# Kernel optimization log

Hardware: AMD Instinct MI355X
Metric: run time of the kernel (lower is better)

Reference implementation:

```python
import jax, jax.numpy as jnp
import numpy as np

B, K, U = 4096, 512, 3
P, LIFT, HID, NSUB = 5, 32, 128, 10
RATE_LO, RATE_HI = 0.01, 3.0
BASAL_LO, BASAL_HI = 0.0, 0.3


def _xavier(key, shape):
    fan_in, fan_out = shape[1], shape[0]
    lim = np.sqrt(6.0 / (fan_in + fan_out))
    return jax.random.uniform(key, shape, jnp.float32, -lim, lim)


def setup_inputs() -> dict:
    key = jax.random.key(0)
    ks = jax.random.split(key, 10)
    return {
        "y0": jax.random.uniform(ks[0], (B, P), jnp.float32),
        "u_seq": jax.random.uniform(ks[1], (B, K, U), jnp.float32),
        "dt_seq": jax.random.uniform(ks[2], (B, K), jnp.float32),
        # lift: Linear(in_u+P -> LIFT)
        "Wl": _xavier(ks[3], (LIFT, U + P)),
        "bl": jnp.zeros((LIFT,), jnp.float32),
        # GRU (single layer): weight_ih (3H, LIFT), weight_hh (3H, H)
        "W_ih": _xavier(ks[4], (3 * HID, LIFT)),
        "b_ih": jnp.zeros((3 * HID,), jnp.float32),
        "W_hh": _xavier(ks[5], (3 * HID, HID)),
        "b_hh": jnp.zeros((3 * HID,), jnp.float32),
        # head: Linear(H -> 13)
        "Wh": _xavier(ks[6], (13, HID)),
        "bh": jnp.zeros((13,), jnp.float32),
        # bolus-to-state jump matrix (in_u, P)
        "u_to_y_jump": 0.1 * jax.random.uniform(ks[7], (U, P), jnp.float32),
    }


def _rhs(y, theta):
    # y: (B,5) [A,D,G,J,M]; theta: (B,13) [kf1..4, kr1..4, kj1..5]
    A, D, G, J, M = (y[:, i] for i in range(5))
    kf1, kf2, kf3, kf4, kr1, kr2, kr3, kr4, kj1, kj2, kj3, kj4, kj5 = (
        theta[:, i] for i in range(13))
    dA = -kf1 * A + kr1 * D + kj1
    dD = kf1 * A - kr1 * D - kf2 * D + kr2 * G + kj2
    dG = kf2 * D - kr2 * G - kf3 * G + kr3 * J + kj3
    dJ = kf3 * G - kr3 * J - kf4 * J + kr4 * M + kj4
    dM = kf4 * J - kr4 * M + kj5
    return jnp.stack([dA, dD, dG, dJ, dM], axis=-1)


def _rk4(y, h, theta):
    # h: (B,1) substep size
    k1 = _rhs(y, theta)
    k2 = _rhs(y + 0.5 * h * k1, theta)
    k3 = _rhs(y + 0.5 * h * k2, theta)
    k4 = _rhs(y + h * k3, theta)
    return jnp.maximum(y + h / 6.0 * (k1 + 2.0 * k2 + 2.0 * k3 + k4), 0.0)


def reference(y0, u_seq, dt_seq, Wl, bl, W_ih, b_ih, W_hh, b_hh, Wh, bh, u_to_y_jump):
    Bb = y0.shape[0]
    hid = W_hh.shape[1]

    def step(carry, inp):
        y_prev, hst = carry
        u_k, dt_k = inp  # (B,U), (B,)
        feat = jnp.concatenate([u_k, jax.lax.stop_gradient(y_prev)], axis=-1)
        x = jax.nn.silu(feat @ Wl.T + bl)
        # PyTorch GRUCell math
        gx = x @ W_ih.T + b_ih
        gh = hst @ W_hh.T + b_hh
        gxr, gxz, gxn = jnp.split(gx, 3, axis=-1)
        ghr, ghz, ghn = jnp.split(gh, 3, axis=-1)
        r = jax.nn.sigmoid(gxr + ghr)
        zg = jax.nn.sigmoid(gxz + ghz)
        n = jnp.tanh(gxn + r * ghn)
        h_new = (1.0 - zg) * n + zg * hst
        raw = h_new @ Wh.T + bh
        rates = RATE_LO + (RATE_HI - RATE_LO) * jax.nn.sigmoid(raw[:, 0:8])
        basal = BASAL_LO + (BASAL_HI - BASAL_LO) * jax.nn.sigmoid(raw[:, 8:13])
        theta = jnp.concatenate([rates, basal], axis=-1)
        y = y_prev + u_k @ u_to_y_jump
        hsub = (dt_k / float(NSUB))[:, None]
        for _ in range(NSUB):
            y = _rk4(y, hsub, theta)
        return (y, h_new), (y, theta)

    y_init = y0 + 0.01
    h0 = jnp.zeros((Bb, hid), dtype=y0.dtype)
    # scan over time: (K,B,...)
    _, (ys, thetas) = jax.lax.scan(
        step, (y_init, h0), (u_seq.transpose(1, 0, 2), dt_seq.T))
    y_out = ys.transpose(1, 0, 2)        # (B,K,P)
    theta_out = thetas.transpose(1, 0, 2)  # (B,K,13)
    return y_out, theta_out
```

## Files before the change

### kernel.cpp

```cpp
#include <hip/hip_runtime.h>
#include <cstdint>
#include <cstddef>


#define KTOT 512
#define BB   16

typedef _Float16 half8 __attribute__((ext_vector_type(8)));
typedef float    f32x4 __attribute__((ext_vector_type(4)));

struct __align__(16) Smem {
  _Float16 hf16[BB][136];
  _Float16 xls[BB][32];
  float brz[256];
  float bnx[128];
  float bnh[128];
  float bhv[16];
  float theta[BB][14];
  float yst[BB][8];
  float ust[2][BB][4];
  float dtst[2][BB];
};

__device__ __forceinline__ float sigm(float x)     { return 1.f / (1.f + __expf(-x)); }
__device__ __forceinline__ float tanhfast(float x) { return 1.f - 2.f / (1.f + __expf(2.f * x)); }

template<int CTRL>
__device__ __forceinline__ float dppf(float x) {
  return __int_as_float(__builtin_amdgcn_mov_dpp(__float_as_int(x), CTRL, 0xf, 0xf, true));
}
#define QP_PLUS  0x39
#define QP_MINUS 0x93
#define QB0 0x00
#define QB1 0x55
#define QB2 0xAA
#define QB3 0xFF

#define MATMUL(Yr, Y4r, Xr, X4r, ALPHA) do {                                  \
  float xm_[5], xp_[5];                                                       \
  _Pragma("unroll")                                                           \
  for (int j_ = 0; j_ < 5; j_++) {                                            \
    xm_[j_] = dppf<QP_MINUS>(Xr[j_]);                                         \
    xp_[j_] = dppf<QP_PLUS >(Xr[j_]);                                         \
  }                                                                           \
  _Pragma("unroll")                                                           \
  for (int j_ = 0; j_ < 5; j_++) {                                            \
    const float ac_ = Zl*xm_[j_] + Zd*Xr[j_] + Zu*xp_[j_] + Zu4*X4r[j_];      \
    const float a4_ = Z43*Xr[j_] + Z44*X4r[j_];                               \
    Yr[j_]  = ((j_ == s_) ? 1.f : 0.f) + (ALPHA)*ac_;                         \
    Y4r[j_] = ((j_ == 4 ) ? 1.f : 0.f) + (ALPHA)*a4_;                         \
  } } while (0)

__global__ __launch_bounds__(512, 2) void rnn_scan_kernel(
    const float* __restrict__ y0,    const float* __restrict__ u_seq,
    const float* __restrict__ dt_sq, const float* __restrict__ Wl,
    const float* __restrict__ bl,    const float* __restrict__ W_ih,
    const float* __restrict__ b_ih,  const float* __restrict__ W_hh,
    const float* __restrict__ b_hh,  const float* __restrict__ Wh,
    const float* __restrict__ bh,    const float* __restrict__ jmp,
    float* __restrict__ y_out, float* __restrict__ th_out)
{
  __shared__ Smem sm;
  const int t   = threadIdx.x;
  const int w   = t >> 6;
  const int l   = t & 63;
  const int n16 = l & 15;
  const int q   = l >> 4;
  const int B0  = blockIdx.x * BB;

  if (t < 256) sm.brz[t] = b_ih[t] + b_hh[t];
  if (t < 128) { sm.bnx[t] = b_ih[256+t]; sm.bnh[t] = b_hh[256+t]; }
  if (t < 16)  sm.bhv[t] = (t < 13) ? bh[t] : 0.f;
  if (t >= 256 && t < 384) { const int b = (t-256) >> 3, i = (t-256) & 7;
    sm.yst[b][i] = (i < 5) ? (y0[(size_t)(B0+b)*5 + i] + 0.01f) : 0.f; }
  if (t >= 384 && t < 432) { const int b = (t-384)/3, c = (t-384) - ((t-384)/3)*3;
    sm.ust[0][b][c] = u_seq[((size_t)(B0+b)*KTOT + 0)*3 + c]; }
  if (t >= 432 && t < 448) sm.dtst[0][t-432] = dt_sq[(size_t)(B0+(t-432))*KTOT + 0];

  const int lb = t >> 5;
  const int lo = t & 31;
  float wlc[8];
  #pragma unroll
  for (int c = 0; c < 8; c++) wlc[c] = Wl[lo*8 + c];
  const float blv = bl[lo];

  half8 whf[4];
  #pragma unroll
  for (int ks = 0; ks < 4; ks++)
    #pragma unroll
    for (int i = 0; i < 8; i++) {
      const int kk = ks*32 + q*8 + i;
      whf[ks][i] = (n16 < 13) ? (_Float16)Wh[n16*128 + kk] : (_Float16)0.f;
    }

  const int jR = w*16 + n16;
  const int jZ = jR + 128, jN = jR + 256;
  half8 wihR, wihZ, wihN, whhR[4], whhZ[4], whhN[4];
  #pragma unroll
  for (int i = 0; i < 8; i++) {
    const int kk = q*8 + i;
    wihR[i] = (_Float16)W_ih[jR*32 + kk];
    wihZ[i] = (_Float16)W_ih[jZ*32 + kk];
    wihN[i] = (_Float16)W_ih[jN*32 + kk];
  }
  #pragma unroll
  for (int ks = 0; ks < 4; ks++)
    #pragma unroll
    for (int i = 0; i < 8; i++) {
      const int kk = ks*32 + q*8 + i;
      whhR[ks][i] = (_Float16)W_hh[jR*128 + kk];
      whhZ[ks][i] = (_Float16)W_hh[jZ*128 + kk];
      whhN[ks][i] = (_Float16)W_hh[jN*128 + kk];
    }

  float hreg[4] = {0.f, 0.f, 0.f, 0.f};
  const f32x4 zero4 = {0.f, 0.f, 0.f, 0.f};
  f32x4 accPreR = zero4, accPreZ = zero4, accPreN = zero4;

  const int s_ = l & 3, b4 = l >> 2;
  const float jr0 = jmp[0*5 + s_], jr1 = jmp[1*5 + s_], jr2 = jmp[2*5 + s_];
  const float j40 = (s_==3) ? jmp[4]  : 0.f;
  const float j41 = (s_==3) ? jmp[9]  : 0.f;
  const float j42 = (s_==3) ? jmp[14] : 0.f;

  const int yb = t/5, yi = t - (t/5)*5;
  float* yo_base = y_out + ((size_t)(B0 + (yb & 15))*KTOT)*5 + yi;
  const int ts = (t >= 80) ? (t - 80) : 0;
  const int tb = ts/13, tn = ts - (ts/13)*13;
  float* th_base = th_out + ((size_t)(B0 + (tb & 15))*KTOT)*13 + tn;
  const int upb = l/3, upc = l - (l/3)*3;

  __syncthreads();

  const float br  = sm.brz[jR];
  const float bz  = sm.brz[128 + jR];
  const float bx  = sm.bnx[jR];
  const float bn  = sm.bnh[jR];
  const float bb_ = sm.bhv[n16];

  #pragma unroll 1
  for (int k = 0; k < KTOT; k++) {
    const int buf  = k & 1;
    const int nbuf = (k + 1) & 1;
    const int kp   = (k + 1 < KTOT) ? (k + 1) : (KTOT - 1);

    {
      const f32x4 uu = *(const f32x4*)&sm.ust[buf][lb][0];
      const f32x4 ya = *(const f32x4*)&sm.yst[lb][0];
      const f32x4 yc = *(const f32x4*)&sm.yst[lb][4];
      const float a = blv
        + uu[0]*wlc[0] + uu[1]*wlc[1] + uu[2]*wlc[2]
        + ya[0]*wlc[3] + ya[1]*wlc[4] + ya[2]*wlc[5] + ya[3]*wlc[6]
        + yc[0]*wlc[7];
      sm.xls[lb][lo] = (_Float16)(a * sigm(a));
    }
    __syncthreads();

    if (k > 0) {
      if (t < 80)        yo_base[(size_t)(k-1)*5]  = sm.yst[yb][yi];
      else if (t < 288)  th_base[(size_t)(k-1)*13] = sm.theta[tb][tn];
    }
    {
      const half8 xf = *(const half8*)&sm.xls[n16][q*8];
      const f32x4 accR  = __builtin_amdgcn_mfma_f32_16x16x32_f16(xf, wihR, accPreR, 0,0,0);
      const f32x4 accZ  = __builtin_amdgcn_mfma_f32_16x16x32_f16(xf, wihZ, accPreZ, 0,0,0);
      const f32x4 accXN = __builtin_amdgcn_mfma_f32_16x16x32_f16(xf, wihN, zero4,   0,0,0);
      #pragma unroll
      for (int rg = 0; rg < 4; rg++) {
        const float r  = sigm(accR[rg] + br);
        const float z  = sigm(accZ[rg] + bz);
        const float nn = tanhfast(accXN[rg] + bx + r*(accPreN[rg] + bn));
        const float ho = hreg[rg];
        const float hn = nn + z*(ho - nn);
        hreg[rg] = hn;
        sm.hf16[q*4 + rg][jR] = (_Float16)hn;
      }
    }
    __syncthreads();

    float pref_u = 0.f, pref_dt = 0.f;
    if (w == 1 && l < 48)
      pref_u = u_seq[((size_t)(B0 + upb)*KTOT + kp)*3 + upc];
    if (w == 2 && l < 16)
      pref_dt = dt_sq[(size_t)(B0 + l)*KTOT + kp];

    half8 hfrag[4];
    #pragma unroll
    for (int ks = 0; ks < 4; ks++)
      hfrag[ks] = *(const half8*)&sm.hf16[n16][ks*32 + q*8];

    accPreR = zero4; accPreZ = zero4; accPreN = zero4;
    #pragma unroll
    for (int ks = 0; ks < 4; ks++) {
      accPreR = __builtin_amdgcn_mfma_f32_16x16x32_f16(hfrag[ks], whhR[ks], accPreR, 0,0,0);
      accPreZ = __builtin_amdgcn_mfma_f32_16x16x32_f16(hfrag[ks], whhZ[ks], accPreZ, 0,0,0);
      accPreN = __builtin_amdgcn_mfma_f32_16x16x32_f16(hfrag[ks], whhN[ks], accPreN, 0,0,0);
    }

    if (w == 0) {
      f32x4 accH = zero4;
      #pragma unroll
      for (int ks = 0; ks < 4; ks++)
        accH = __builtin_amdgcn_mfma_f32_16x16x32_f16(hfrag[ks], whf[ks], accH, 0,0,0);
      #pragma unroll
      for (int rg = 0; rg < 4; rg++) {
        const float sg  = sigm(accH[rg] + bb_);
        const float thv = (n16 < 8) ? (0.01f + 2.99f*sg) : (0.3f*sg);
        if (n16 < 13) sm.theta[q*4 + rg][n16] = thv;
      }
      const float* th = sm.theta[b4];
      const float dt = sm.dtst[buf][b4];
      const float h  = dt * 0.1f;
      const float thm = th[s_ ? (s_ - 1) : 0];
      const float Zl  = s_ ? h*thm : 0.f;
      const float krs = s_ ? th[3 + s_] : 0.f;
      const float Zd  = -h*(th[s_] + krs);
      const float Zur = h*th[4 + s_];
      const float Zu  = (s_ < 3) ? Zur : 0.f;
      const float Zu4 = (s_ == 3) ? Zur : 0.f;
      const float Z43 = h*th[3];
      const float Z44 = -h*th[7];
      const float c0 = th[8], c1 = th[9], c2 = th[10], c3 = th[11], c4 = th[12];
      float Xa[5], Xa4[5], Xb[5], Xb4[5];
      #pragma unroll
      for (int j = 0; j < 5; j++) {
        const float zr = (j == s_) ? Zd : ((j == s_ + 1) ? Zur : ((j + 1 == s_) ? Zl : 0.f));
        Xa[j] = ((j == s_) ? 1.f : 0.f) + 0.25f*zr;
      }
      Xa4[0] = 0.f; Xa4[1] = 0.f; Xa4[2] = 0.f;
      Xa4[3] = 0.25f*Z43; Xa4[4] = 1.f + 0.25f*Z44;
      MATMUL(Xb, Xb4, Xa, Xa4, (1.f/3.f));
      MATMUL(Xa, Xa4, Xb, Xb4, 0.5f);
      const float bv  = h*(Xa[0]*c0 + Xa[1]*c1 + Xa[2]*c2 + Xa[3]*c3 + Xa[4]*c4);
      const float bv4 = h*(Xa4[0]*c0 + Xa4[1]*c1 + Xa4[2]*c2 + Xa4[3]*c3 + Xa4[4]*c4);
      MATMUL(Xb, Xb4, Xa, Xa4, 1.f);
      const float uu0 = sm.ust[buf][b4][0], uu1 = sm.ust[buf][b4][1], uu2 = sm.ust[buf][b4][2];
      float y  = sm.yst[b4][s_] + uu0*jr0 + uu1*jr1 + uu2*jr2;
      float y4 = sm.yst[b4][4]  + uu0*j40 + uu1*j41 + uu2*j42;
      #pragma unroll
      for (int ss = 0; ss < 10; ss++) {
        const float v0 = dppf<QB0>(y), v1 = dppf<QB1>(y),
                    v2 = dppf<QB2>(y), v3 = dppf<QB3>(y);
        const float v4 = dppf<QB3>(y4);
        const float yn  = fmaxf(bv  + Xb[0]*v0 + Xb[1]*v1 + Xb[2]*v2 + Xb[3]*v3 + Xb[4]*v4, 0.f);
        const float y4n = fmaxf(bv4 + Xb4[0]*v0 + Xb4[1]*v1 + Xb4[2]*v2 + Xb4[3]*v3 + Xb4[4]*v4, 0.f);
        y = yn; y4 = y4n;
      }
      sm.yst[b4][s_] = y;
      if (s_ == 3) sm.yst[b4][4] = y4;
    }
    if (w == 1 && l < 48) sm.ust[nbuf][upb][upc] = pref_u;
    if (w == 2 && l < 16) sm.dtst[nbuf][l] = pref_dt;
    __syncthreads();
  }

  if (t < 80)        yo_base[(size_t)(KTOT-1)*5]  = sm.yst[yb][yi];
  else if (t < 288)  th_base[(size_t)(KTOT-1)*13] = sm.theta[tb][tn];
}

extern "C" void kernel_launch(void* const* d_in, const int* in_sizes, int n_in,
                              void* d_out, int out_size, void* d_ws, size_t ws_size,
                              hipStream_t stream) {
  const float* y0     = (const float*)d_in[0];
  const float* u_seq  = (const float*)d_in[1];
  const float* dt_sq  = (const float*)d_in[2];
  const float* Wl     = (const float*)d_in[3];
  const float* bl     = (const float*)d_in[4];
  const float* W_ih   = (const float*)d_in[5];
  const float* b_ih   = (const float*)d_in[6];
  const float* W_hh   = (const float*)d_in[7];
  const float* b_hh   = (const float*)d_in[8];
  const float* Wh     = (const float*)d_in[9];
  const float* bh     = (const float*)d_in[10];
  const float* jmp    = (const float*)d_in[11];
  float* y_out  = (float*)d_out;
  float* th_out = y_out + (size_t)4096 * KTOT * 5;
  rnn_scan_kernel<<<256, 512, 0, stream>>>(
      y0, u_seq, dt_sq, Wl, bl, W_ih, b_ih, W_hh, b_hh, Wh, bh, jmp, y_out, th_out);
}
```

Baseline: 1.474 ms.

## Buffer 16 timesteps of outputs in LDS ring and flush with vector stores

Replaces the per-timestep scalar global stores of y and theta with a double-buffered shared-memory ring holding 16 steps. Every 16 steps the idle waves flush the previous half as contiguous 16-byte stores, overlapping with wave 0's ODE work. The change also splits the RK4 update's dot products into a shallower FMA tree to cut dependency latency. It costs more LDS per block, which could reduce occupancy, and relies on the output rows being 16-byte aligned.

```diff
diff --git a/kernel.cpp b/kernel.cpp
--- a/kernel.cpp
+++ b/kernel.cpp
@@ -12,11 +12,12 @@
 struct __align__(16) Smem {
   _Float16 hf16[BB][136];
   _Float16 xls[BB][32];
+  float yring[2][BB][16][5];
+  float thring[2][BB][16][13];
   float brz[256];
   float bnx[128];
   float bnh[128];
   float bhv[16];
-  float theta[BB][14];
   float yst[BB][8];
   float ust[2][BB][4];
   float dtst[2][BB];
@@ -73,7 +74,7 @@
   if (t < 16)  sm.bhv[t] = (t < 13) ? bh[t] : 0.f;
   if (t >= 256 && t < 384) { const int b = (t-256) >> 3, i = (t-256) & 7;
     sm.yst[b][i] = (i < 5) ? (y0[(size_t)(B0+b)*5 + i] + 0.01f) : 0.f; }
-  if (t >= 384 && t < 432) { const int b = (t-384)/3, c = (t-384) - ((t-384)/3)*3;
+  if (t >= 384 && t < 432) { const int idx = t-384, b = idx/3, c = idx - (idx/3)*3;
     sm.ust[0][b][c] = u_seq[((size_t)(B0+b)*KTOT + 0)*3 + c]; }
   if (t >= 432 && t < 448) sm.dtst[0][t-432] = dt_sq[(size_t)(B0+(t-432))*KTOT + 0];
 
@@ -123,11 +124,6 @@
   const float j41 = (s_==3) ? jmp[9]  : 0.f;
   const float j42 = (s_==3) ? jmp[14] : 0.f;
 
-  const int yb = t/5, yi = t - (t/5)*5;
-  float* yo_base = y_out + ((size_t)(B0 + (yb & 15))*KTOT)*5 + yi;
-  const int ts = (t >= 80) ? (t - 80) : 0;
-  const int tb = ts/13, tn = ts - (ts/13)*13;
-  float* th_base = th_out + ((size_t)(B0 + (tb & 15))*KTOT)*13 + tn;
   const int upb = l/3, upc = l - (l/3)*3;
 
   __syncthreads();
@@ -156,10 +152,6 @@
     }
     __syncthreads();
 
-    if (k > 0) {
-      if (t < 80)        yo_base[(size_t)(k-1)*5]  = sm.yst[yb][yi];
-      else if (t < 288)  th_base[(size_t)(k-1)*13] = sm.theta[tb][tn];
-    }
     {
       const half8 xf = *(const half8*)&sm.xls[n16][q*8];
       const f32x4 accR  = __builtin_amdgcn_mfma_f32_16x16x32_f16(xf, wihR, accPreR, 0,0,0);
@@ -198,6 +190,7 @@
     }
 
     if (w == 0) {
+      const int km = k & 15, hh = (k >> 4) & 1;
       f32x4 accH = zero4;
       #pragma unroll
       for (int ks = 0; ks < 4; ks++)
@@ -206,9 +199,9 @@
       for (int rg = 0; rg < 4; rg++) {
         const float sg  = sigm(accH[rg] + bb_);
         const float thv = (n16 < 8) ? (0.01f + 2.99f*sg) : (0.3f*sg);
-        if (n16 < 13) sm.theta[q*4 + rg][n16] = thv;
-      }
-      const float* th = sm.theta[b4];
+        if (n16 < 13) sm.thring[hh][q*4 + rg][km][n16] = thv;
+      }
+      const float* th = &sm.thring[hh][b4][km][0];
       const float dt = sm.dtst[buf][b4];
       const float h  = dt * 0.1f;
       const float thm = th[s_ ? (s_ - 1) : 0];
@@ -242,20 +235,67 @@
         const float v0 = dppf<QB0>(y), v1 = dppf<QB1>(y),
                     v2 = dppf<QB2>(y), v3 = dppf<QB3>(y);
         const float v4 = dppf<QB3>(y4);
-        const float yn  = fmaxf(bv  + Xb[0]*v0 + Xb[1]*v1 + Xb[2]*v2 + Xb[3]*v3 + Xb[4]*v4, 0.f);
-        const float y4n = fmaxf(bv4 + Xb4[0]*v0 + Xb4[1]*v1 + Xb4[2]*v2 + Xb4[3]*v3 + Xb4[4]*v4, 0.f);
+        const float a1 = fmaf(Xb[0],  v0, bv);
+        const float a2 = fmaf(Xb[2],  v2, Xb[1]*v1);
+        const float a3 = fmaf(Xb[4],  v4, Xb[3]*v3);
+        const float b1 = fmaf(Xb4[0], v0, bv4);
+        const float b2 = fmaf(Xb4[2], v2, Xb4[1]*v1);
+        const float b3 = fmaf(Xb4[4], v4, Xb4[3]*v3);
+        const float yn  = fmaxf(a1 + (a2 + a3), 0.f);
+        const float y4n = fmaxf(b1 + (b2 + b3), 0.f);
         y = yn; y4 = y4n;
       }
       sm.yst[b4][s_] = y;
-      if (s_ == 3) sm.yst[b4][4] = y4;
+      sm.yring[hh][b4][km][s_] = y;
+      if (s_ == 3) { sm.yst[b4][4] = y4; sm.yring[hh][b4][km][4] = y4; }
+    } else {
+      if ((k & 15) == 0 && k >= 16) {
+        const int hf = ((k >> 4) & 1) ^ 1;
+        const int kb = k - 16;
+        const int idx = t - 64;
+        #pragma unroll
+        for (int rep = 0; rep < 3; rep++) {
+          const int o = idx + rep*448;
+          if (o < 1152) {
+            if (o < 320) {
+              const int b = o/20, j = o - b*20;
+              *(f32x4*)&y_out[((size_t)(B0 + b)*KTOT + kb)*5 + j*4] =
+                  *(const f32x4*)((const float*)&sm.yring[hf][b][0][0] + j*4);
+            } else {
+              const int o2 = o - 320;
+              const int b = o2/52, j = o2 - b*52;
+              *(f32x4*)&th_out[((size_t)(B0 + b)*KTOT + kb)*13 + j*4] =
+                  *(const f32x4*)((const float*)&sm.thring[hf][b][0][0] + j*4);
+            }
+          }
+        }
+      }
     }
     if (w == 1 && l < 48) sm.ust[nbuf][upb][upc] = pref_u;
     if (w == 2 && l < 16) sm.dtst[nbuf][l] = pref_dt;
     __syncthreads();
   }
 
-  if (t < 80)        yo_base[(size_t)(KTOT-1)*5]  = sm.yst[yb][yi];
-  else if (t < 288)  th_base[(size_t)(KTOT-1)*13] = sm.theta[tb][tn];
+  {
+    const int kb = KTOT - 16;
+    const int hf = ((KTOT >> 4) & 1) ^ 1;
+    #pragma unroll
+    for (int rep = 0; rep < 3; rep++) {
+      const int o = t + rep*512;
+      if (o < 1152) {
+        if (o < 320) {
+          const int b = o/20, j = o - b*20;
+          *(f32x4*)&y_out[((size_t)(B0 + b)*KTOT + kb)*5 + j*4] =
+              *(const f32x4*)((const float*)&sm.yring[hf][b][0][0] + j*4);
+        } else {
+          const int o2 = o - 320;
+          const int b = o2/52, j = o2 - b*52;
+          *(f32x4*)&th_out[((size_t)(B0 + b)*KTOT + kb)*13 + j*4] =
+              *(const f32x4*)((const float*)&sm.thring[hf][b][0][0] + j*4);
+        }
+      }
+    }
+  }
 }
 
 extern "C" void kernel_launch(void* const* d_in, const int* in_sizes, int n_in,
```

Measured after the change: 1.374 ms. 1.07x faster.
